# Optimization experiments

Measured on AMD Instinct MI355X. Metric: run time of the kernel, lower is better.

The kernel has to match this reference:

```python
import jax, jax.numpy as jnp
import numpy as np

N_NODES = 50000
N_EDGES = 1600000
DIM_IN = 64
DIM = 64
DIM_OUT = 32
N_GRAPHS = 64
DELTA = 2.5749
BN_EPS = 1e-5


def _lin(x, W, b):
    return x @ W.T + b


def _pna_conv(x, src, dst, mlp_W, mlp_b, W1, b1, W2, b2):
    # GINConv with overridden PNA aggregate: nn(x + aggr(x_j))
    msgs = x[src]                                               # [E, d]
    n = x.shape[0]
    sums = jax.ops.segment_sum(msgs, dst, num_segments=n)       # [N, d]
    maxs = jax.ops.segment_max(msgs, dst, num_segments=n)
    cnt = jax.ops.segment_sum(jnp.ones((msgs.shape[0], 1), msgs.dtype), dst,
                              num_segments=n)                   # [N, 1]
    means = sums / cnt
    var = jax.nn.relu(jax.ops.segment_sum(msgs * msgs, dst, num_segments=n) / cnt
                      - means * means)
    aggr = jnp.concatenate([sums, maxs, means, var], axis=1)    # [N, 4d]
    comb = jnp.concatenate([aggr, (cnt / DELTA) * aggr, (DELTA / cnt) * aggr],
                           axis=1)                              # [N, 12d]
    a = _lin(comb, mlp_W, mlp_b)                                # [N, d]
    h = x + a                                                   # (1+eps)*x + aggr, eps=0
    return _lin(jax.nn.relu(_lin(h, W1, b1)), W2, b2)


def _bn(x, g, b):
    # BatchNorm1d with batch statistics (training-mode stats, biased var)
    m = x.mean(axis=0)
    v = ((x - m) ** 2).mean(axis=0)
    return g * (x - m) / jnp.sqrt(v + BN_EPS) + b


def setup_inputs() -> dict:
    key = jax.random.key(0)
    ks = jax.random.split(key, 32)
    x = jax.random.normal(ks[0], (N_NODES, DIM_IN), dtype=jnp.float32)
    src = jax.random.randint(ks[1], (N_EDGES,), 0, N_NODES)
    dst = jax.random.randint(ks[2], (N_EDGES,), 0, N_NODES)
    # guarantee every node has >=1 incoming edge (original divides by bincount)
    dst = dst.at[:N_NODES].set(jnp.arange(N_NODES))
    edge_index = jnp.stack([src, dst]).astype(jnp.int32)
    batch = jnp.sort(jax.random.randint(ks[3], (N_NODES,), 0, N_GRAPHS)).astype(jnp.int32)

    def w(k, shape):
        return jax.random.normal(k, shape, dtype=jnp.float32) * 0.1

    d = {"x": x, "edge_index": edge_index, "batch": batch}
    i = 4
    for c in ("c1", "c2", "c3"):
        d[f"{c}_mlp_W"] = w(ks[i], (DIM, DIM * 12)); i += 1
        d[f"{c}_mlp_b"] = jnp.zeros((DIM,), jnp.float32)
        d[f"{c}_W1"] = w(ks[i], (DIM, DIM)); i += 1
        d[f"{c}_b1"] = jnp.zeros((DIM,), jnp.float32)
        d[f"{c}_W2"] = w(ks[i], (DIM, DIM)); i += 1
        d[f"{c}_b2"] = jnp.zeros((DIM,), jnp.float32)
    for b in ("bn1", "bn2", "bn3"):
        d[f"{b}_g"] = jnp.ones((DIM,), jnp.float32)
        d[f"{b}_b"] = jnp.zeros((DIM,), jnp.float32)
    d["fc1_W"] = w(ks[i], (DIM, DIM)); i += 1
    d["fc1_b"] = jnp.zeros((DIM,), jnp.float32)
    d["fc2_W"] = w(ks[i], (DIM_OUT, DIM)); i += 1
    d["fc2_b"] = jnp.zeros((DIM_OUT,), jnp.float32)
    return d


def reference(x, edge_index, batch,
              c1_mlp_W, c1_mlp_b, c1_W1, c1_b1, c1_W2, c1_b2, bn1_g, bn1_b,
              c2_mlp_W, c2_mlp_b, c2_W1, c2_b1, c2_W2, c2_b2, bn2_g, bn2_b,
              c3_mlp_W, c3_mlp_b, c3_W1, c3_b1, c3_W2, c3_b2, bn3_g, bn3_b,
              fc1_W, fc1_b, fc2_W, fc2_b):
    src, dst = edge_index[0], edge_index[1]
    h = jax.nn.relu(_pna_conv(x, src, dst, c1_mlp_W, c1_mlp_b, c1_W1, c1_b1, c1_W2, c1_b2))
    h = _bn(h, bn1_g, bn1_b)
    h = jax.nn.relu(_pna_conv(h, src, dst, c2_mlp_W, c2_mlp_b, c2_W1, c2_b1, c2_W2, c2_b2))
    h = _bn(h, bn2_g, bn2_b)
    h = jax.nn.relu(_pna_conv(h, src, dst, c3_mlp_W, c3_mlp_b, c3_W1, c3_b1, c3_W2, c3_b2))
    h = _bn(h, bn3_g, bn3_b)
    g = jax.ops.segment_sum(h, batch, num_segments=N_GRAPHS)   # global_add_pool
    g = jax.nn.relu(_lin(g, fc1_W, fc1_b))                     # dropout disabled (eval)
    g = _lin(g, fc2_W, fc2_b)
    return jax.nn.log_softmax(g, axis=-1)
```

## Files before the change

kernel.cpp:

```cpp
#include <hip/hip_runtime.h>

#define NN 50000
#define NE 1600000
#define DD 64
#define NGRAPH 64
#define DOUT 32
#define DELTA_F 2.5749f
#define BN_EPS_F 1e-5f

typedef unsigned short ushort;
typedef __attribute__((ext_vector_type(8))) short short8;
typedef __attribute__((ext_vector_type(4))) float floatx4;

static __device__ __forceinline__ float blo(unsigned u) {
    return __uint_as_float(u << 16);
}
static __device__ __forceinline__ float bhi(unsigned u) {
    return __uint_as_float(u & 0xFFFF0000u);
}
static __device__ __forceinline__ float bu2f(ushort u) {
    return __uint_as_float(((unsigned)u) << 16);
}
static __device__ __forceinline__ ushort f2bu(float f) {
    unsigned u = __float_as_uint(f);
    unsigned r = (u + 0x7FFF + ((u >> 16) & 1)) >> 16;
    return (ushort)r;
}
static __device__ __forceinline__ unsigned pk(float a, float b) {
    return ((unsigned)f2bu(b) << 16) | (unsigned)f2bu(a);
}

__global__ void k_prep(const float* __restrict__ x, ushort* __restrict__ XH,
                       const float* __restrict__ w0, const float* __restrict__ w1,
                       const float* __restrict__ w2,
                       const float* __restrict__ a0, const float* __restrict__ a1,
                       const float* __restrict__ a2, const float* __restrict__ a3,
                       const float* __restrict__ a4, const float* __restrict__ a5,
                       ushort* __restrict__ Wb, float* __restrict__ Wsm,
                       int* __restrict__ counts, float* __restrict__ bnstat,
                       float* __restrict__ gpool) {
    int i = blockIdx.x * 256 + threadIdx.x;
    if (i < NN) counts[i] = 0;
    if (i < 384) bnstat[i] = 0.f;
    if (i < NGRAPH * DD) gpool[i] = 0.f;
    if (i < NN * 16) {
        float4 v = *(const float4*)(x + (size_t)i * 4);
        ushort4 h;
        h.x = f2bu(v.x); h.y = f2bu(v.y); h.z = f2bu(v.z); h.w = f2bu(v.w);
        *(ushort4*)(XH + (size_t)i * 4) = h;
    }
    if (i < 3 * 65536) {
        int layer = i / 65536, r = i % 65536;
        const float* w = (layer == 0) ? w0 : ((layer == 1) ? w1 : w2);
        int c = r / 16384, r2 = r % 16384;
        int kb = r2 >> 11, r3 = r2 & 2047;
        int t = r3 >> 9, r4 = r3 & 511;
        int l = r4 >> 3, j = r4 & 7;
        int k = kb * 32 + (l >> 4) * 8 + j;
        int o = t * 16 + (l & 15);
        int g = (c == 0) ? 0 : ((c == 3) ? 2 : 1);
        float wv = w[o * 768 + g * 256 + k];
        ushort h = f2bu(wv);
        Wb[i] = (c == 2) ? f2bu(wv - bu2f(h)) : h;
    } else if (i < 3 * 65536 + 6 * 4096) {
        int r2 = i - 3 * 65536;
        int l = r2 >> 12, r = r2 & 4095;
        const float* w = (l == 0) ? a0 : (l == 1) ? a1 : (l == 2) ? a2
                       : (l == 3) ? a3 : (l == 4) ? a4 : a5;
        int o = r >> 6, j = r & 63;
        Wsm[l * 4096 + j * 64 + o] = w[r];
    }
}

__global__ void k_rank(const int* __restrict__ dst, int* __restrict__ counts,
                       int* __restrict__ rank) {
    int e = blockIdx.x * 256 + threadIdx.x;
    if (e < NE) rank[e] = atomicAdd(&counts[dst[e]], 1);
}

__global__ void k_scan_a(const int* __restrict__ counts, int* __restrict__ blockSums) {
    __shared__ int red[256];
    int tid = threadIdx.x;
    int gid = blockIdx.x * 256 + tid;
    int v = (gid < NN) ? counts[gid] : 0;
    red[tid] = v;
    __syncthreads();
    for (int s = 128; s > 0; s >>= 1) {
        if (tid < s) red[tid] += red[tid + s];
        __syncthreads();
    }
    if (tid == 0) blockSums[blockIdx.x] = red[0];
}

__global__ void k_scan_b(const int* __restrict__ blockSums, int* __restrict__ blockBase,
                         const int* __restrict__ batch, int* __restrict__ gcnt) {
    __shared__ int sh[256];
    int tid = threadIdx.x;
    int v = (tid < 196) ? blockSums[tid] : 0;
    sh[tid] = v;
    __syncthreads();
    for (int off = 1; off < 256; off <<= 1) {
        int t = (tid >= off) ? sh[tid - off] : 0;
        __syncthreads();
        sh[tid] += t;
        __syncthreads();
    }
    blockBase[tid] = sh[tid] - v;
    if (tid < NGRAPH) {
        auto lb = [&](int g) {
            int lo = 0, hi = NN;
            while (lo < hi) {
                int mid = (lo + hi) >> 1;
                if (batch[mid] < g) lo = mid + 1; else hi = mid;
            }
            return lo;
        };
        gcnt[tid] = lb(tid + 1) - lb(tid);
    }
}

__global__ void k_scan_c(const int* __restrict__ counts, const int* __restrict__ blockBase,
                         int* __restrict__ row_ptr) {
    __shared__ int sh[256];
    int tid = threadIdx.x;
    int gid = blockIdx.x * 256 + tid;
    int v = (gid < NN) ? counts[gid] : 0;
    sh[tid] = v;
    __syncthreads();
    for (int off = 1; off < 256; off <<= 1) {
        int t = (tid >= off) ? sh[tid - off] : 0;
        __syncthreads();
        sh[tid] += t;
        __syncthreads();
    }
    int excl = blockBase[blockIdx.x] + sh[tid] - v;
    if (gid <= NN) row_ptr[gid] = excl;
}

__global__ void k_place(const int* __restrict__ src, const int* __restrict__ dst,
                        const int* __restrict__ rank, const int* __restrict__ row_ptr,
                        int* __restrict__ csr_src) {
    int e = blockIdx.x * 256 + threadIdx.x;
    if (e < NE) csr_src[row_ptr[dst[e]] + rank[e]] = src[e];
}

#define MBIAS(i) aux[i]
#define B1V(i)   aux[64 + (i)]
#define B2V(i)   aux[128 + (i)]
#define DEGV(m)  aux[192 + (m)]
#define AFFS(i)  aux[224 + (i)]
#define AFFB(i)  aux[288 + (i)]

__global__ __launch_bounds__(256, 4) void k_fused(
    const ushort* __restrict__ XHin, ushort* __restrict__ XHout,
    const int* __restrict__ row_ptr, const int* __restrict__ csr_src,
    const ushort* __restrict__ Wbh,
    const float* __restrict__ mlp_b,
    const float* __restrict__ W1t, const float* __restrict__ b1,
    const float* __restrict__ W2t, const float* __restrict__ b2,
    const float* __restrict__ affstat, const float* __restrict__ affg,
    const float* __restrict__ affb,
    float* __restrict__ bnstat,
    const int* __restrict__ batch, float* __restrict__ gpool, int do_pool) {
    __shared__ __align__(16) char smem[27136];
    ushort* const Agh = (ushort*)smem;
    ushort* const Agl = (ushort*)(smem + 12800);
    float* const aux = (float*)(smem + 25600);
    int* const ibatch = (int*)(smem + 27008);
    float* const hsf = (float*)smem;

    const int tid = threadIdx.x;
    const int node0 = blockIdx.x * 32;

    if (tid < 64) {
        MBIAS(tid) = mlp_b[tid];
        B1V(tid) = b1[tid];
        B2V(tid) = b2[tid];
        float A = 1.f, Bv = 0.f;
        if (affstat) {
            float mean = affstat[tid] * (1.f / NN);
            float var = fmaxf(affstat[64 + tid] * (1.f / NN) - mean * mean, 0.f);
            float inv = rsqrtf(var + BN_EPS_F);
            A = affg[tid] * inv;
            Bv = affb[tid] - mean * A;
        }
        AFFS(tid) = A;
        AFFB(tid) = Bv;
    }
    if (tid < 32) {
        int node = node0 + tid;
        ibatch[tid] = (do_pool && node < NN) ? batch[node] : -1;
    }
    __syncthreads();

    {
        const int l8 = tid & 7;
        const int m = tid >> 3;
        const int node = node0 + m;
        const int f0 = l8 * 8;
        const ushort* Xp = XHin + f0;

        float s[8], q[8], mx[8];
#pragma unroll
        for (int i = 0; i < 8; ++i) { s[i] = 0.f; q[i] = 0.f; mx[i] = -3.402823466e38f; }

        auto acc8 = [&](const uint4& rr) {
            float v0 = blo(rr.x), v1 = bhi(rr.x);
            float v2 = blo(rr.y), v3 = bhi(rr.y);
            float v4 = blo(rr.z), v5 = bhi(rr.z);
            float v6 = blo(rr.w), v7 = bhi(rr.w);
            s[0] += v0; q[0] = fmaf(v0, v0, q[0]); mx[0] = fmaxf(mx[0], v0);
            s[1] += v1; q[1] = fmaf(v1, v1, q[1]); mx[1] = fmaxf(mx[1], v1);
            s[2] += v2; q[2] = fmaf(v2, v2, q[2]); mx[2] = fmaxf(mx[2], v2);
            s[3] += v3; q[3] = fmaf(v3, v3, q[3]); mx[3] = fmaxf(mx[3], v3);
            s[4] += v4; q[4] = fmaf(v4, v4, q[4]); mx[4] = fmaxf(mx[4], v4);
            s[5] += v5; q[5] = fmaf(v5, v5, q[5]); mx[5] = fmaxf(mx[5], v5);
            s[6] += v6; q[6] = fmaf(v6, v6, q[6]); mx[6] = fmaxf(mx[6], v6);
            s[7] += v7; q[7] = fmaf(v7, v7, q[7]); mx[7] = fmaxf(mx[7], v7);
        };

        int beg = 0, end = 0;
        if (node < NN) { beg = row_ptr[node]; end = row_ptr[node + 1]; }
        const int deg = end - beg;
        const int nb = (deg + 3) >> 2;

        uint4 ra[4], rb[4];
        int ia[4];
        if (nb > 0) {
#pragma unroll
            for (int j = 0; j < 4; ++j) {
                int e = beg + j;
                ia[j] = csr_src[(e < end) ? e : end - 1];
            }
#pragma unroll
            for (int j = 0; j < 4; ++j)
                ra[j] = *(const uint4*)(Xp + (size_t)ia[j] * 64);
            if (nb > 1) {
#pragma unroll
                for (int j = 0; j < 4; ++j) {
                    int e = beg + 4 + j;
                    ia[j] = csr_src[(e < end) ? e : end - 1];
                }
            }
        }
        for (int t = 0; t < nb; ++t) {
            if (t + 1 < nb) {
#pragma unroll
                for (int j = 0; j < 4; ++j)
                    rb[j] = *(const uint4*)(Xp + (size_t)ia[j] * 64);
            }
            if (t + 2 < nb) {
                int b2e = beg + (t + 2) * 4;
#pragma unroll
                for (int j = 0; j < 4; ++j) {
                    int e = b2e + j;
                    ia[j] = csr_src[(e < end) ? e : end - 1];
                }
            }
            int cnt = end - (beg + t * 4);
            if (cnt >= 4) {
#pragma unroll
                for (int j = 0; j < 4; ++j) acc8(ra[j]);
            } else {
#pragma unroll
                for (int j = 0; j < 4; ++j) if (j < cnt) acc8(ra[j]);
            }
            if (t + 1 < nb) {
#pragma unroll
                for (int j = 0; j < 4; ++j) ra[j] = rb[j];
            }
        }

        float cdeg = (node < NN) ? (float)deg : 1.f;
        float rc = 1.0f / cdeg;
        float var[8];
#pragma unroll
        for (int i = 0; i < 8; ++i) {
            float mean = s[i] * rc;
            var[i] = fmaxf(q[i] * rc - mean * mean, 0.f);
            if (node >= NN) { mx[i] = 0.f; var[i] = 0.f; }
        }
#pragma unroll
        for (int i = 0; i < 8; ++i) {
            float Af = AFFS(f0 + i), Bf = AFFB(f0 + i);
            s[i] = Af * s[i] + cdeg * Bf;
            mx[i] = Af * mx[i] + Bf;
            var[i] = Af * Af * var[i];
        }
        ushort* dh = Agh + m * 200 + f0;
        ushort* dl = Agl + m * 200 + f0;
        auto emit8 = [&](const float* v, int off) {
            ushort h0 = f2bu(v[0]), h1 = f2bu(v[1]), h2 = f2bu(v[2]), h3 = f2bu(v[3]);
            ushort h4 = f2bu(v[4]), h5 = f2bu(v[5]), h6 = f2bu(v[6]), h7 = f2bu(v[7]);
            uint4 hv;
            hv.x = (unsigned)h0 | ((unsigned)h1 << 16);
            hv.y = (unsigned)h2 | ((unsigned)h3 << 16);
            hv.z = (unsigned)h4 | ((unsigned)h5 << 16);
            hv.w = (unsigned)h6 | ((unsigned)h7 << 16);
            uint4 lv;
            lv.x = pk(v[0] - bu2f(h0), v[1] - bu2f(h1));
            lv.y = pk(v[2] - bu2f(h2), v[3] - bu2f(h3));
            lv.z = pk(v[4] - bu2f(h4), v[5] - bu2f(h5));
            lv.w = pk(v[6] - bu2f(h6), v[7] - bu2f(h7));
            *(uint4*)(dh + off) = hv;
            *(uint4*)(dl + off) = lv;
        };
        emit8(s, 0);
        emit8(mx, 64);
        emit8(var, 128);
        if (l8 == 0) DEGV(m) = cdeg;
    }
    __syncthreads();

    const int ln = tid & 63, wvi = tid >> 6;
    const int quad = ln >> 4, l16 = ln & 15;
    const int mtile = wvi >> 1;
    const int nt0 = (wvi & 1) * 2;

    const ushort* ArowH = Agh + (mtile * 16 + l16) * 200 + quad * 8;
    const ushort* ArowL = Agl + (mtile * 16 + l16) * 200 + quad * 8;
    short8 afh[6], afl[6];
#pragma unroll
    for (int i = 0; i < 6; ++i) {
        const int off = (i >> 1) * 64 + (i & 1) * 32;
        afh[i] = *(const short8*)(ArowH + off);
        afl[i] = *(const short8*)(ArowL + off);
    }
    __syncthreads();

#pragma unroll
    for (int nti = 0; nti < 2; ++nti) {
        const int nt = nt0 + nti;
        floatx4 aA0 = (floatx4){0.f, 0.f, 0.f, 0.f};
        floatx4 aB0 = (floatx4){0.f, 0.f, 0.f, 0.f};
        floatx4 aA1 = (floatx4){0.f, 0.f, 0.f, 0.f};
        floatx4 aB1 = (floatx4){0.f, 0.f, 0.f, 0.f};
        floatx4 aA2 = (floatx4){0.f, 0.f, 0.f, 0.f};
        floatx4 aB2 = (floatx4){0.f, 0.f, 0.f, 0.f};
#pragma unroll
        for (int kb = 0; kb < 8; ++kb) {
            const int am = (kb < 4) ? kb : ((kb < 6) ? (kb - 4) : (kb - 2));
            const int base = ((kb * 4 + nt) * 512) + ln * 8;
            short8 w0 = *(const short8*)(Wbh + base);
            short8 w1h = *(const short8*)(Wbh + 16384 + base);
            short8 w2 = *(const short8*)(Wbh + 3 * 16384 + base);
            if (kb == 4 || kb == 5) {
                aB0 = __builtin_amdgcn_mfma_f32_16x16x32_bf16(afh[am], w0, aB0, 0, 0, 0);
                aB1 = __builtin_amdgcn_mfma_f32_16x16x32_bf16(afh[am], w1h, aB1, 0, 0, 0);
                aB2 = __builtin_amdgcn_mfma_f32_16x16x32_bf16(afh[am], w2, aB2, 0, 0, 0);
            } else {
                short8 w1l = *(const short8*)(Wbh + 2 * 16384 + base);
                aA0 = __builtin_amdgcn_mfma_f32_16x16x32_bf16(afh[am], w0, aA0, 0, 0, 0);
                aA1 = __builtin_amdgcn_mfma_f32_16x16x32_bf16(afh[am], w1h, aA1, 0, 0, 0);
                aA1 = __builtin_amdgcn_mfma_f32_16x16x32_bf16(afl[am], w1h, aA1, 0, 0, 0);
                aA1 = __builtin_amdgcn_mfma_f32_16x16x32_bf16(afh[am], w1l, aA1, 0, 0, 0);
                aA2 = __builtin_amdgcn_mfma_f32_16x16x32_bf16(afh[am], w2, aA2, 0, 0, 0);
            }
        }
#pragma unroll
        for (int r = 0; r < 4; ++r) {
            int m = mtile * 16 + quad * 4 + r;
            float dg = DEGV(m), rcd = 1.f / dg;
            float cA2 = DELTA_F * rcd;
            float cB2 = DELTA_F * rcd * rcd;
            float cA1 = dg * (1.0f / DELTA_F);
            int n = nt * 16 + l16;
            hsf[n * 34 + m] = aA0[r] + rcd * aB0[r]
                            + cA2 * aA2[r] + cB2 * aB2[r]
                            + cA1 * aA1[r] + (1.0f / DELTA_F) * aB1[r];
        }
    }
    __syncthreads();

    const int tx = tid & 15, ty = tid >> 4;
    const int o0 = tx * 4, n0 = ty * 2;
#pragma unroll
    for (int ni = 0; ni < 2; ++ni) {
        int n = n0 + ni;
        int node = node0 + n;
        float xa4[4] = {0.f, 0.f, 0.f, 0.f};
        if (node < NN) {
            ushort4 hx = *(const ushort4*)(XHin + (size_t)node * DD + o0);
            xa4[0] = AFFS(o0 + 0) * bu2f(hx.x) + AFFB(o0 + 0);
            xa4[1] = AFFS(o0 + 1) * bu2f(hx.y) + AFFB(o0 + 1);
            xa4[2] = AFFS(o0 + 2) * bu2f(hx.z) + AFFB(o0 + 2);
            xa4[3] = AFFS(o0 + 3) * bu2f(hx.w) + AFFB(o0 + 3);
        }
#pragma unroll
        for (int oi = 0; oi < 4; ++oi) {
            int idx = (o0 + oi) * 34 + n;
            hsf[idx] = hsf[idx] + xa4[oi] + MBIAS(o0 + oi);
        }
    }
    __syncthreads();

    const float2* const hs2 = (const float2*)hsf;
    float l1[8];
#pragma unroll
    for (int i = 0; i < 8; ++i) l1[i] = 0.f;
#pragma unroll 4
    for (int j = 0; j < 64; ++j) {
        float2 a = hs2[j * 17 + ty];
        const float4 wv4 = *(const float4*)(W1t + j * 64 + o0);
        l1[0] += a.x * wv4.x; l1[1] += a.x * wv4.y; l1[2] += a.x * wv4.z; l1[3] += a.x * wv4.w;
        l1[4] += a.y * wv4.x; l1[5] += a.y * wv4.y; l1[6] += a.y * wv4.z; l1[7] += a.y * wv4.w;
    }
    __syncthreads();
#pragma unroll
    for (int ni = 0; ni < 2; ++ni)
#pragma unroll
        for (int oi = 0; oi < 4; ++oi)
            hsf[(o0 + oi) * 34 + n0 + ni] = fmaxf(l1[ni * 4 + oi] + B1V(o0 + oi), 0.f);
    __syncthreads();

    float l2[8];
#pragma unroll
    for (int i = 0; i < 8; ++i) l2[i] = 0.f;
#pragma unroll 4
    for (int j = 0; j < 64; ++j) {
        float2 a = hs2[j * 17 + ty];
        const float4 wv4 = *(const float4*)(W2t + j * 64 + o0);
        l2[0] += a.x * wv4.x; l2[1] += a.x * wv4.y; l2[2] += a.x * wv4.z; l2[3] += a.x * wv4.w;
        l2[4] += a.y * wv4.x; l2[5] += a.y * wv4.y; l2[6] += a.y * wv4.z; l2[7] += a.y * wv4.w;
    }
    __syncthreads();
#pragma unroll
    for (int ni = 0; ni < 2; ++ni) {
        int node = node0 + n0 + ni;
        float4 yv;
        yv.x = fmaxf(l2[ni * 4 + 0] + B2V(o0 + 0), 0.f);
        yv.y = fmaxf(l2[ni * 4 + 1] + B2V(o0 + 1), 0.f);
        yv.z = fmaxf(l2[ni * 4 + 2] + B2V(o0 + 2), 0.f);
        yv.w = fmaxf(l2[ni * 4 + 3] + B2V(o0 + 3), 0.f);
        if (node < NN && XHout) {
            ushort4 h;
            h.x = f2bu(yv.x); h.y = f2bu(yv.y);
            h.z = f2bu(yv.z); h.w = f2bu(yv.w);
            *(ushort4*)(XHout + (size_t)node * DD + o0) = h;
        }
        hsf[(o0 + 0) * 34 + n0 + ni] = yv.x;
        hsf[(o0 + 1) * 34 + n0 + ni] = yv.y;
        hsf[(o0 + 2) * 34 + n0 + ni] = yv.z;
        hsf[(o0 + 3) * 34 + n0 + ni] = yv.w;
    }
    __syncthreads();

    if (tid < 64) {
        float s = 0.f, sq = 0.f;
        float pacc = 0.f;
        int curg = ibatch[0];
        int lim = NN - node0;
        if (lim > 32) lim = 32;
        for (int n = 0; n < lim; ++n) {
            float v = hsf[tid * 34 + n];
            s += v;
            sq += v * v;
            if (do_pool) {
                int g = ibatch[n];
                if (g != curg) {
                    atomicAdd(&gpool[(size_t)curg * DD + tid], pacc);
                    pacc = 0.f;
                    curg = g;
                }
                pacc += v;
            }
        }
        if (do_pool && curg >= 0)
            atomicAdd(&gpool[(size_t)curg * DD + tid], pacc);
        atomicAdd(&bnstat[tid], s);
        atomicAdd(&bnstat[64 + tid], sq);
    }
}

__global__ __launch_bounds__(256) void k_head(const float* __restrict__ gpool,
                                              const float* __restrict__ bs3,
                                              const float* __restrict__ g3,
                                              const float* __restrict__ b3,
                                              const int* __restrict__ gcnt,
                                              const float* __restrict__ fc1W, const float* __restrict__ fc1b,
                                              const float* __restrict__ fc2W, const float* __restrict__ fc2b,
                                              float* __restrict__ out) {
    __shared__ float sh[12640];
    float* const gs = sh;
    float* const w1t = sh + 4096;
    float* const z1s = sh + 8256;
    float* const b1s = sh + 12416;
    float* const b2s = sh + 12480;
    float* const sc3 = sh + 12512;
    float* const shf3 = sh + 12576;
    float* const w2t = sh;
    float* const z2s = sh + 4096;

    int tid = threadIdx.x;
    if (tid < 64) {
        float mean = bs3[tid] * (1.f / NN);
        float var = fmaxf(bs3[64 + tid] * (1.f / NN) - mean * mean, 0.f);
        float inv = rsqrtf(var + BN_EPS_F);
        float A = g3[tid] * inv;
        sc3[tid] = A;
        shf3[tid] = b3[tid] - mean * A;
    }
    __syncthreads();
    for (int i = tid; i < 4096; i += 256) {
        int o = i >> 6, j = i & 63;
        gs[i] = sc3[j] * gpool[i] + shf3[j] * (float)gcnt[o];
        w1t[j * 65 + o] = fc1W[i];
    }
    if (tid < 64) b1s[tid] = fc1b[tid];
    if (tid < 32) b2s[tid] = fc2b[tid];
    __syncthreads();
    {
        int tx = tid & 15, ty = tid >> 4, o0 = tx * 4, g0 = ty * 4;
        float acc[16];
#pragma unroll
        for (int i = 0; i < 16; ++i) acc[i] = 0.f;
        for (int j = 0; j < 64; ++j) {
            float w0 = w1t[j * 65 + o0 + 0], w1 = w1t[j * 65 + o0 + 1];
            float w2 = w1t[j * 65 + o0 + 2], w3 = w1t[j * 65 + o0 + 3];
#pragma unroll
            for (int gi = 0; gi < 4; ++gi) {
                float a = gs[(g0 + gi) * 64 + j];
                acc[gi * 4 + 0] += a * w0; acc[gi * 4 + 1] += a * w1;
                acc[gi * 4 + 2] += a * w2; acc[gi * 4 + 3] += a * w3;
            }
        }
        __syncthreads();
#pragma unroll
        for (int gi = 0; gi < 4; ++gi)
#pragma unroll
            for (int oi = 0; oi < 4; ++oi)
                z1s[(g0 + gi) * 65 + o0 + oi] = fmaxf(acc[gi * 4 + oi] + b1s[o0 + oi], 0.f);
    }
    for (int i = tid; i < 2048; i += 256) {
        int o = i >> 6, j = i & 63;
        w2t[j * 33 + o] = fc2W[i];
    }
    __syncthreads();
    {
        int tx = tid & 7, ty = tid >> 3, o0 = tx * 4, g0 = ty * 2;
        float acc[8];
#pragma unroll
        for (int i = 0; i < 8; ++i) acc[i] = 0.f;
        for (int j = 0; j < 64; ++j) {
            float w0 = w2t[j * 33 + o0 + 0], w1 = w2t[j * 33 + o0 + 1];
            float w2 = w2t[j * 33 + o0 + 2], w3 = w2t[j * 33 + o0 + 3];
            float a0 = z1s[(g0 + 0) * 65 + j];
            float a1 = z1s[(g0 + 1) * 65 + j];
            acc[0] += a0 * w0; acc[1] += a0 * w1; acc[2] += a0 * w2; acc[3] += a0 * w3;
            acc[4] += a1 * w0; acc[5] += a1 * w1; acc[6] += a1 * w2; acc[7] += a1 * w3;
        }
#pragma unroll
        for (int gi = 0; gi < 2; ++gi)
#pragma unroll
            for (int oi = 0; oi < 4; ++oi)
                z2s[(g0 + gi) * 33 + o0 + oi] = acc[gi * 4 + oi] + b2s[o0 + oi];
    }
    __syncthreads();
    if (tid < 64) {
        float m = -3.402823466e38f;
        for (int c = 0; c < DOUT; ++c) m = fmaxf(m, z2s[tid * 33 + c]);
        float s = 0.f;
        for (int c = 0; c < DOUT; ++c) s += expf(z2s[tid * 33 + c] - m);
        float lse = m + logf(s);
        for (int c = 0; c < DOUT; ++c)
            out[tid * DOUT + c] = z2s[tid * 33 + c] - lse;
    }
}

extern "C" void kernel_launch(void* const* d_in, const int* in_sizes, int n_in,
                              void* d_out, int out_size, void* d_ws, size_t ws_size,
                              hipStream_t stream) {
    const float* x = (const float*)d_in[0];
    const int* ei = (const int*)d_in[1];
    const int* src = ei;
    const int* dst = ei + NE;
    const int* batch = (const int*)d_in[2];
    const float *mlpW[3], *mlpB[3], *w1[3], *bb1[3], *w2[3], *bb2[3], *bng[3], *bnb[3];
    for (int l = 0; l < 3; ++l) {
        mlpW[l] = (const float*)d_in[3 + 6 * l];
        mlpB[l] = (const float*)d_in[4 + 6 * l];
        w1[l]   = (const float*)d_in[5 + 6 * l];
        bb1[l]  = (const float*)d_in[6 + 6 * l];
        w2[l]   = (const float*)d_in[7 + 6 * l];
        bb2[l]  = (const float*)d_in[8 + 6 * l];
        bng[l]  = (const float*)d_in[21 + 2 * l];
        bnb[l]  = (const float*)d_in[22 + 2 * l];
    }
    const float* fc1W = (const float*)d_in[27];
    const float* fc1b = (const float*)d_in[28];
    const float* fc2W = (const float*)d_in[29];
    const float* fc2b = (const float*)d_in[30];
    float* out = (float*)d_out;

    char* ws = (char*)d_ws;
    size_t off = 0;
    auto alloc = [&](size_t bytes) -> void* {
        void* p = ws + off;
        off = (off + bytes + 511) & ~(size_t)511;
        return p;
    };
    int* counts    = (int*)alloc((size_t)NN * 4);
    int* row_ptr   = (int*)alloc((size_t)(NN + 1) * 4);
    int* rank      = (int*)alloc((size_t)NE * 4);
    int* blockSums = (int*)alloc(256 * 4);
    int* blockBase = (int*)alloc(256 * 4);
    int* csr_src   = (int*)alloc((size_t)NE * 4);
    ushort* XHA    = (ushort*)alloc((size_t)NN * DD * 2);
    ushort* XHB    = (ushort*)alloc((size_t)NN * DD * 2);
    ushort* Wb     = (ushort*)alloc((size_t)3 * 65536 * 2);
    float* Wsm     = (float*)alloc((size_t)6 * 4096 * 4);
    float* bnstat  = (float*)alloc(384 * 4);
    float* gpool   = (float*)alloc((size_t)NGRAPH * DD * 4);
    int* gcnt      = (int*)alloc(NGRAPH * 4);
    (void)ws_size; (void)in_sizes; (void)n_in; (void)out_size;

    k_prep<<<3125, 256, 0, stream>>>(x, XHA,
                                     mlpW[0], mlpW[1], mlpW[2],
                                     w1[0], w2[0], w1[1], w2[1], w1[2], w2[2],
                                     Wb, Wsm, counts, bnstat, gpool);
    k_rank<<<6250, 256, 0, stream>>>(dst, counts, rank);
    k_scan_a<<<196, 256, 0, stream>>>(counts, blockSums);
    k_scan_b<<<1, 256, 0, stream>>>(blockSums, blockBase, batch, gcnt);
    k_scan_c<<<196, 256, 0, stream>>>(counts, blockBase, row_ptr);
    k_place<<<6250, 256, 0, stream>>>(src, dst, rank, row_ptr, csr_src);

    k_fused<<<1563, 256, 0, stream>>>(XHA, XHB, row_ptr, csr_src,
                                      Wb, mlpB[0],
                                      Wsm, bb1[0], Wsm + 4096, bb2[0],
                                      nullptr, nullptr, nullptr,
                                      bnstat, batch, gpool, 0);
    k_fused<<<1563, 256, 0, stream>>>(XHB, XHA, row_ptr, csr_src,
                                      Wb + 65536, mlpB[1],
                                      Wsm + 2 * 4096, bb1[1], Wsm + 3 * 4096, bb2[1],
                                      bnstat, bng[0], bnb[0],
                                      bnstat + 128, batch, gpool, 0);
    k_fused<<<1563, 256, 0, stream>>>(XHA, nullptr, row_ptr, csr_src,
                                      Wb + 2 * 65536, mlpB[2],
                                      Wsm + 4 * 4096, bb1[2], Wsm + 5 * 4096, bb2[2],
                                      bnstat + 128, bng[1], bnb[1],
                                      bnstat + 256, batch, gpool, 1);
    k_head<<<1, 256, 0, stream>>>(gpool, bnstat + 256, bng[2], bnb[2], gcnt,
                                  fc1W, fc1b, fc2W, fc2b, out);
}
```

Baseline: 493.4 us.

## Double threads per fused block and vectorize edge rank/place kernels

```diff
diff --git a/kernel.cpp b/kernel.cpp
--- a/kernel.cpp
+++ b/kernel.cpp
@@ -74,8 +74,16 @@
 
 __global__ void k_rank(const int* __restrict__ dst, int* __restrict__ counts,
                        int* __restrict__ rank) {
-    int e = blockIdx.x * 256 + threadIdx.x;
-    if (e < NE) rank[e] = atomicAdd(&counts[dst[e]], 1);
+    int i = blockIdx.x * 256 + threadIdx.x;
+    if (i < NE / 4) {
+        int4 d = ((const int4*)dst)[i];
+        int4 r;
+        r.x = atomicAdd(&counts[d.x], 1);
+        r.y = atomicAdd(&counts[d.y], 1);
+        r.z = atomicAdd(&counts[d.z], 1);
+        r.w = atomicAdd(&counts[d.w], 1);
+        ((int4*)rank)[i] = r;
+    }
 }
 
 __global__ void k_scan_a(const int* __restrict__ counts, int* __restrict__ blockSums) {
@@ -140,8 +148,16 @@
 __global__ void k_place(const int* __restrict__ src, const int* __restrict__ dst,
                         const int* __restrict__ rank, const int* __restrict__ row_ptr,
                         int* __restrict__ csr_src) {
-    int e = blockIdx.x * 256 + threadIdx.x;
-    if (e < NE) csr_src[row_ptr[dst[e]] + rank[e]] = src[e];
+    int i = blockIdx.x * 256 + threadIdx.x;
+    if (i < NE / 4) {
+        int4 s4 = ((const int4*)src)[i];
+        int4 d4 = ((const int4*)dst)[i];
+        int4 r4 = ((const int4*)rank)[i];
+        csr_src[row_ptr[d4.x] + r4.x] = s4.x;
+        csr_src[row_ptr[d4.y] + r4.y] = s4.y;
+        csr_src[row_ptr[d4.z] + r4.z] = s4.z;
+        csr_src[row_ptr[d4.w] + r4.w] = s4.w;
+    }
 }
 
 #define MBIAS(i) aux[i]
@@ -151,7 +167,7 @@
 #define AFFS(i)  aux[224 + (i)]
 #define AFFB(i)  aux[288 + (i)]
 
-__global__ __launch_bounds__(256, 4) void k_fused(
+__global__ __launch_bounds__(512, 6) void k_fused(
     const ushort* __restrict__ XHin, ushort* __restrict__ XHout,
     const int* __restrict__ row_ptr, const int* __restrict__ csr_src,
     const ushort* __restrict__ Wbh,
@@ -194,29 +210,23 @@
     __syncthreads();
 
     {
-        const int l8 = tid & 7;
-        const int m = tid >> 3;
+        const int l16g = tid & 15;
+        const int m = tid >> 4;
         const int node = node0 + m;
-        const int f0 = l8 * 8;
+        const int f0 = l16g * 4;
         const ushort* Xp = XHin + f0;
 
-        float s[8], q[8], mx[8];
-#pragma unroll
-        for (int i = 0; i < 8; ++i) { s[i] = 0.f; q[i] = 0.f; mx[i] = -3.402823466e38f; }
-
-        auto acc8 = [&](const uint4& rr) {
+        float s[4], q[4], mx[4];
+#pragma unroll
+        for (int i = 0; i < 4; ++i) { s[i] = 0.f; q[i] = 0.f; mx[i] = -3.402823466e38f; }
+
+        auto acc4 = [&](const uint2& rr) {
             float v0 = blo(rr.x), v1 = bhi(rr.x);
             float v2 = blo(rr.y), v3 = bhi(rr.y);
-            float v4 = blo(rr.z), v5 = bhi(rr.z);
-            float v6 = blo(rr.w), v7 = bhi(rr.w);
             s[0] += v0; q[0] = fmaf(v0, v0, q[0]); mx[0] = fmaxf(mx[0], v0);
             s[1] += v1; q[1] = fmaf(v1, v1, q[1]); mx[1] = fmaxf(mx[1], v1);
             s[2] += v2; q[2] = fmaf(v2, v2, q[2]); mx[2] = fmaxf(mx[2], v2);
             s[3] += v3; q[3] = fmaf(v3, v3, q[3]); mx[3] = fmaxf(mx[3], v3);
-            s[4] += v4; q[4] = fmaf(v4, v4, q[4]); mx[4] = fmaxf(mx[4], v4);
-            s[5] += v5; q[5] = fmaf(v5, v5, q[5]); mx[5] = fmaxf(mx[5], v5);
-            s[6] += v6; q[6] = fmaf(v6, v6, q[6]); mx[6] = fmaxf(mx[6], v6);
-            s[7] += v7; q[7] = fmaf(v7, v7, q[7]); mx[7] = fmaxf(mx[7], v7);
         };
 
         int beg = 0, end = 0;
@@ -224,7 +234,7 @@
         const int deg = end - beg;
         const int nb = (deg + 3) >> 2;
 
-        uint4 ra[4], rb[4];
+        uint2 ra[4], rb[4];
         int ia[4];
         if (nb > 0) {
 #pragma unroll
@@ -234,7 +244,7 @@
             }
 #pragma unroll
             for (int j = 0; j < 4; ++j)
-                ra[j] = *(const uint4*)(Xp + (size_t)ia[j] * 64);
+                ra[j] = *(const uint2*)(Xp + (size_t)ia[j] * 64);
             if (nb > 1) {
 #pragma unroll
                 for (int j = 0; j < 4; ++j) {
@@ -247,7 +257,7 @@
             if (t + 1 < nb) {
 #pragma unroll
                 for (int j = 0; j < 4; ++j)
-                    rb[j] = *(const uint4*)(Xp + (size_t)ia[j] * 64);
+                    rb[j] = *(const uint2*)(Xp + (size_t)ia[j] * 64);
             }
             if (t + 2 < nb) {
                 int b2e = beg + (t + 2) * 4;
@@ -260,10 +270,10 @@
             int cnt = end - (beg + t * 4);
             if (cnt >= 4) {
 #pragma unroll
-                for (int j = 0; j < 4; ++j) acc8(ra[j]);
+                for (int j = 0; j < 4; ++j) acc4(ra[j]);
             } else {
 #pragma unroll
-                for (int j = 0; j < 4; ++j) if (j < cnt) acc8(ra[j]);
+                for (int j = 0; j < 4; ++j) if (j < cnt) acc4(ra[j]);
             }
             if (t + 1 < nb) {
 #pragma unroll
@@ -273,15 +283,15 @@
 
         float cdeg = (node < NN) ? (float)deg : 1.f;
         float rc = 1.0f / cdeg;
-        float var[8];
-#pragma unroll
-        for (int i = 0; i < 8; ++i) {
+        float var[4];
+#pragma unroll
+        for (int i = 0; i < 4; ++i) {
             float mean = s[i] * rc;
             var[i] = fmaxf(q[i] * rc - mean * mean, 0.f);
             if (node >= NN) { mx[i] = 0.f; var[i] = 0.f; }
         }
 #pragma unroll
-        for (int i = 0; i < 8; ++i) {
+        for (int i = 0; i < 4; ++i) {
             float Af = AFFS(f0 + i), Bf = AFFB(f0 + i);
             s[i] = Af * s[i] + cdeg * Bf;
             mx[i] = Af * mx[i] + Bf;
@@ -289,48 +299,40 @@
         }
         ushort* dh = Agh + m * 200 + f0;
         ushort* dl = Agl + m * 200 + f0;
-        auto emit8 = [&](const float* v, int off) {
+        auto emit4 = [&](const float* v, int off) {
             ushort h0 = f2bu(v[0]), h1 = f2bu(v[1]), h2 = f2bu(v[2]), h3 = f2bu(v[3]);
-            ushort h4 = f2bu(v[4]), h5 = f2bu(v[5]), h6 = f2bu(v[6]), h7 = f2bu(v[7]);
-            uint4 hv;
+            uint2 hv;
             hv.x = (unsigned)h0 | ((unsigned)h1 << 16);
             hv.y = (unsigned)h2 | ((unsigned)h3 << 16);
-            hv.z = (unsigned)h4 | ((unsigned)h5 << 16);
-            hv.w = (unsigned)h6 | ((unsigned)h7 << 16);
-            uint4 lv;
+            uint2 lv;
             lv.x = pk(v[0] - bu2f(h0), v[1] - bu2f(h1));
             lv.y = pk(v[2] - bu2f(h2), v[3] - bu2f(h3));
-            lv.z = pk(v[4] - bu2f(h4), v[5] - bu2f(h5));
-            lv.w = pk(v[6] - bu2f(h6), v[7] - bu2f(h7));
-            *(uint4*)(dh + off) = hv;
-            *(uint4*)(dl + off) = lv;
+            *(uint2*)(dh + off) = hv;
+            *(uint2*)(dl + off) = lv;
         };
-        emit8(s, 0);
-        emit8(mx, 64);
-        emit8(var, 128);
-        if (l8 == 0) DEGV(m) = cdeg;
+        emit4(s, 0);
+        emit4(mx, 64);
+        emit4(var, 128);
+        if (l16g == 0) DEGV(m) = cdeg;
     }
     __syncthreads();
 
     const int ln = tid & 63, wvi = tid >> 6;
     const int quad = ln >> 4, l16 = ln & 15;
-    const int mtile = wvi >> 1;
-    const int nt0 = (wvi & 1) * 2;
+    const int mtile = wvi >> 2;
+    const int nt = wvi & 3;
 
     const ushort* ArowH = Agh + (mtile * 16 + l16) * 200 + quad * 8;
     const ushort* ArowL = Agl + (mtile * 16 + l16) * 200 + quad * 8;
-    short8 afh[6], afl[6];
+    short8 afh[6];
 #pragma unroll
     for (int i = 0; i < 6; ++i) {
         const int off = (i >> 1) * 64 + (i & 1) * 32;
         afh[i] = *(const short8*)(ArowH + off);
-        afl[i] = *(const short8*)(ArowL + off);
-    }
-    __syncthreads();
-
-#pragma unroll
-    for (int nti = 0; nti < 2; ++nti) {
-        const int nt = nt0 + nti;
+    }
+    __syncthreads();
+
+    {
         floatx4 aA0 = (floatx4){0.f, 0.f, 0.f, 0.f};
         floatx4 aB0 = (floatx4){0.f, 0.f, 0.f, 0.f};
         floatx4 aA1 = (floatx4){0.f, 0.f, 0.f, 0.f};
@@ -350,9 +352,10 @@
                 aB2 = __builtin_amdgcn_mfma_f32_16x16x32_bf16(afh[am], w2, aB2, 0, 0, 0);
             } else {
                 short8 w1l = *(const short8*)(Wbh + 2 * 16384 + base);
+                short8 al = *(const short8*)(ArowL + ((am >> 1) * 64 + (am & 1) * 32));
                 aA0 = __builtin_amdgcn_mfma_f32_16x16x32_bf16(afh[am], w0, aA0, 0, 0, 0);
                 aA1 = __builtin_amdgcn_mfma_f32_16x16x32_bf16(afh[am], w1h, aA1, 0, 0, 0);
-                aA1 = __builtin_amdgcn_mfma_f32_16x16x32_bf16(afl[am], w1h, aA1, 0, 0, 0);
+                aA1 = __builtin_amdgcn_mfma_f32_16x16x32_bf16(al, w1h, aA1, 0, 0, 0);
                 aA1 = __builtin_amdgcn_mfma_f32_16x16x32_bf16(afh[am], w1l, aA1, 0, 0, 0);
                 aA2 = __builtin_amdgcn_mfma_f32_16x16x32_bf16(afh[am], w2, aA2, 0, 0, 0);
             }
@@ -373,11 +376,9 @@
     __syncthreads();
 
     const int tx = tid & 15, ty = tid >> 4;
-    const int o0 = tx * 4, n0 = ty * 2;
-#pragma unroll
-    for (int ni = 0; ni < 2; ++ni) {
-        int n = n0 + ni;
-        int node = node0 + n;
+    const int o0 = tx * 4;
+    {
+        int node = node0 + ty;
         float xa4[4] = {0.f, 0.f, 0.f, 0.f};
         if (node < NN) {
             ushort4 hx = *(const ushort4*)(XHin + (size_t)node * DD + o0);
@@ -388,60 +389,54 @@
         }
 #pragma unroll
         for (int oi = 0; oi < 4; ++oi) {
-            int idx = (o0 + oi) * 34 + n;
+            int idx = (o0 + oi) * 34 + ty;
             hsf[idx] = hsf[idx] + xa4[oi] + MBIAS(o0 + oi);
         }
     }
     __syncthreads();
 
-    const float2* const hs2 = (const float2*)hsf;
-    float l1[8];
-#pragma unroll
-    for (int i = 0; i < 8; ++i) l1[i] = 0.f;
+    float l1[4];
+#pragma unroll
+    for (int i = 0; i < 4; ++i) l1[i] = 0.f;
 #pragma unroll 4
     for (int j = 0; j < 64; ++j) {
-        float2 a = hs2[j * 17 + ty];
+        float a = hsf[j * 34 + ty];
         const float4 wv4 = *(const float4*)(W1t + j * 64 + o0);
-        l1[0] += a.x * wv4.x; l1[1] += a.x * wv4.y; l1[2] += a.x * wv4.z; l1[3] += a.x * wv4.w;
-        l1[4] += a.y * wv4.x; l1[5] += a.y * wv4.y; l1[6] += a.y * wv4.z; l1[7] += a.y * wv4.w;
-    }
-    __syncthreads();
-#pragma unroll
-    for (int ni = 0; ni < 2; ++ni)
-#pragma unroll
-        for (int oi = 0; oi < 4; ++oi)
-            hsf[(o0 + oi) * 34 + n0 + ni] = fmaxf(l1[ni * 4 + oi] + B1V(o0 + oi), 0.f);
-    __syncthreads();
-
-    float l2[8];
-#pragma unroll
-    for (int i = 0; i < 8; ++i) l2[i] = 0.f;
+        l1[0] += a * wv4.x; l1[1] += a * wv4.y; l1[2] += a * wv4.z; l1[3] += a * wv4.w;
+    }
+    __syncthreads();
+#pragma unroll
+    for (int oi = 0; oi < 4; ++oi)
+        hsf[(o0 + oi) * 34 + ty] = fmaxf(l1[oi] + B1V(o0 + oi), 0.f);
+    __syncthreads();
+
+    float l2[4];
+#pragma unroll
+    for (int i = 0; i < 4; ++i) l2[i] = 0.f;
 #pragma unroll 4
     for (int j = 0; j < 64; ++j) {
-        float2 a = hs2[j * 17 + ty];
+        float a = hsf[j * 34 + ty];
         const float4 wv4 = *(const float4*)(W2t + j * 64 + o0);
-        l2[0] += a.x * wv4.x; l2[1] += a.x * wv4.y; l2[2] += a.x * wv4.z; l2[3] += a.x * wv4.w;
-        l2[4] += a.y * wv4.x; l2[5] += a.y * wv4.y; l2[6] += a.y * wv4.z; l2[7] += a.y * wv4.w;
-    }
-    __syncthreads();
-#pragma unroll
-    for (int ni = 0; ni < 2; ++ni) {
-        int node = node0 + n0 + ni;
+        l2[0] += a * wv4.x; l2[1] += a * wv4.y; l2[2] += a * wv4.z; l2[3] += a * wv4.w;
+    }
+    __syncthreads();
+    {
+        int node = node0 + ty;
         float4 yv;
-        yv.x = fmaxf(l2[ni * 4 + 0] + B2V(o0 + 0), 0.f);
-        yv.y = fmaxf(l2[ni * 4 + 1] + B2V(o0 + 1), 0.f);
-        yv.z = fmaxf(l2[ni * 4 + 2] + B2V(o0 + 2), 0.f);
-        yv.w = fmaxf(l2[ni * 4 + 3] + B2V(o0 + 3), 0.f);
+        yv.x = fmaxf(l2[0] + B2V(o0 + 0), 0.f);
+        yv.y = fmaxf(l2[1] + B2V(o0 + 1), 0.f);
+        yv.z = fmaxf(l2[2] + B2V(o0 + 2), 0.f);
+        yv.w = fmaxf(l2[3] + B2V(o0 + 3), 0.f);
         if (node < NN && XHout) {
             ushort4 h;
             h.x = f2bu(yv.x); h.y = f2bu(yv.y);
             h.z = f2bu(yv.z); h.w = f2bu(yv.w);
             *(ushort4*)(XHout + (size_t)node * DD + o0) = h;
         }
-        hsf[(o0 + 0) * 34 + n0 + ni] = yv.x;
-        hsf[(o0 + 1) * 34 + n0 + ni] = yv.y;
-        hsf[(o0 + 2) * 34 + n0 + ni] = yv.z;
-        hsf[(o0 + 3) * 34 + n0 + ni] = yv.w;
+        hsf[(o0 + 0) * 34 + ty] = yv.x;
+        hsf[(o0 + 1) * 34 + ty] = yv.y;
+        hsf[(o0 + 2) * 34 + ty] = yv.z;
+        hsf[(o0 + 3) * 34 + ty] = yv.w;
     }
     __syncthreads();
 
@@ -618,23 +613,23 @@
                                      mlpW[0], mlpW[1], mlpW[2],
                                      w1[0], w2[0], w1[1], w2[1], w1[2], w2[2],
                                      Wb, Wsm, counts, bnstat, gpool);
-    k_rank<<<6250, 256, 0, stream>>>(dst, counts, rank);
+    k_rank<<<1563, 256, 0, stream>>>(dst, counts, rank);
     k_scan_a<<<196, 256, 0, stream>>>(counts, blockSums);
     k_scan_b<<<1, 256, 0, stream>>>(blockSums, blockBase, batch, gcnt);
     k_scan_c<<<196, 256, 0, stream>>>(counts, blockBase, row_ptr);
-    k_place<<<6250, 256, 0, stream>>>(src, dst, rank, row_ptr, csr_src);
-
-    k_fused<<<1563, 256, 0, stream>>>(XHA, XHB, row_ptr, csr_src,
+    k_place<<<1563, 256, 0, stream>>>(src, dst, rank, row_ptr, csr_src);
+
+    k_fused<<<1563, 512, 0, stream>>>(XHA, XHB, row_ptr, csr_src,
                                       Wb, mlpB[0],
                                       Wsm, bb1[0], Wsm + 4096, bb2[0],
                                       nullptr, nullptr, nullptr,
                                       bnstat, batch, gpool, 0);
-    k_fused<<<1563, 256, 0, stream>>>(XHB, XHA, row_ptr, csr_src,
+    k_fused<<<1563, 512, 0, stream>>>(XHB, XHA, row_ptr, csr_src,
                                       Wb + 65536, mlpB[1],
                                       Wsm + 2 * 4096, bb1[1], Wsm + 3 * 4096, bb2[1],
                                       bnstat, bng[0], bnb[0],
                                       bnstat + 128, batch, gpool, 0);
-    k_fused<<<1563, 256, 0, stream>>>(XHA, nullptr, row_ptr, csr_src,
+    k_fused<<<1563, 512, 0, stream>>>(XHA, nullptr, row_ptr, csr_src,
                                       Wb + 2 * 65536, mlpB[2],
                                       Wsm + 4 * 4096, bb1[2], Wsm + 5 * 4096, bb2[2],
                                       bnstat + 128, bng[1], bnb[1],
```

Measured after the change: 555.4 us. 1.13x slower.

## Move node MLP linears to split-bf16 MFMA and vectorize edge CSR build

Applied to the files above, without the earlier changes.

```diff
diff --git a/kernel.cpp b/kernel.cpp
--- a/kernel.cpp
+++ b/kernel.cpp
@@ -36,7 +36,7 @@
                        const float* __restrict__ a0, const float* __restrict__ a1,
                        const float* __restrict__ a2, const float* __restrict__ a3,
                        const float* __restrict__ a4, const float* __restrict__ a5,
-                       ushort* __restrict__ Wb, float* __restrict__ Wsm,
+                       ushort* __restrict__ Wb, ushort* __restrict__ Wsb,
                        int* __restrict__ counts, float* __restrict__ bnstat,
                        float* __restrict__ gpool) {
     int i = blockIdx.x * 256 + threadIdx.x;
@@ -62,20 +62,37 @@
         float wv = w[o * 768 + g * 256 + k];
         ushort h = f2bu(wv);
         Wb[i] = (c == 2) ? f2bu(wv - bu2f(h)) : h;
-    } else if (i < 3 * 65536 + 6 * 4096) {
-        int r2 = i - 3 * 65536;
-        int l = r2 >> 12, r = r2 & 4095;
-        const float* w = (l == 0) ? a0 : (l == 1) ? a1 : (l == 2) ? a2
-                       : (l == 3) ? a3 : (l == 4) ? a4 : a5;
-        int o = r >> 6, j = r & 63;
-        Wsm[l * 4096 + j * 64 + o] = w[r];
+    } else if (i < 3 * 65536 + 3 * 16384) {
+        int i2 = i - 3 * 65536;
+        int layer = i2 / 16384, r = i2 % 16384;
+        int lin = r >> 13, r2 = r & 8191;
+        int hl = r2 >> 12, r3 = r2 & 4095;
+        int kb = r3 >> 11, r4 = r3 & 2047;
+        int t = r4 >> 9, r5 = r4 & 511;
+        int l = r5 >> 3, j = r5 & 7;
+        int k = kb * 32 + (l >> 4) * 8 + j;
+        int o = t * 16 + (l & 15);
+        const float* w = (lin == 0)
+            ? ((layer == 0) ? a0 : (layer == 1) ? a2 : a4)
+            : ((layer == 0) ? a1 : (layer == 1) ? a3 : a5);
+        float wv = w[o * 64 + k];
+        ushort h = f2bu(wv);
+        Wsb[i2] = hl ? f2bu(wv - bu2f(h)) : h;
     }
 }
 
 __global__ void k_rank(const int* __restrict__ dst, int* __restrict__ counts,
                        int* __restrict__ rank) {
-    int e = blockIdx.x * 256 + threadIdx.x;
-    if (e < NE) rank[e] = atomicAdd(&counts[dst[e]], 1);
+    int i = blockIdx.x * 256 + threadIdx.x;
+    if (i < NE / 4) {
+        int4 d = ((const int4*)dst)[i];
+        int4 r;
+        r.x = atomicAdd(&counts[d.x], 1);
+        r.y = atomicAdd(&counts[d.y], 1);
+        r.z = atomicAdd(&counts[d.z], 1);
+        r.w = atomicAdd(&counts[d.w], 1);
+        ((int4*)rank)[i] = r;
+    }
 }
 
 __global__ void k_scan_a(const int* __restrict__ counts, int* __restrict__ blockSums) {
@@ -140,8 +157,16 @@
 __global__ void k_place(const int* __restrict__ src, const int* __restrict__ dst,
                         const int* __restrict__ rank, const int* __restrict__ row_ptr,
                         int* __restrict__ csr_src) {
-    int e = blockIdx.x * 256 + threadIdx.x;
-    if (e < NE) csr_src[row_ptr[dst[e]] + rank[e]] = src[e];
+    int i = blockIdx.x * 256 + threadIdx.x;
+    if (i < NE / 4) {
+        int4 s4 = ((const int4*)src)[i];
+        int4 d4 = ((const int4*)dst)[i];
+        int4 r4 = ((const int4*)rank)[i];
+        csr_src[row_ptr[d4.x] + r4.x] = s4.x;
+        csr_src[row_ptr[d4.y] + r4.y] = s4.y;
+        csr_src[row_ptr[d4.z] + r4.z] = s4.z;
+        csr_src[row_ptr[d4.w] + r4.w] = s4.w;
+    }
 }
 
 #define MBIAS(i) aux[i]
@@ -154,10 +179,9 @@
 __global__ __launch_bounds__(256, 4) void k_fused(
     const ushort* __restrict__ XHin, ushort* __restrict__ XHout,
     const int* __restrict__ row_ptr, const int* __restrict__ csr_src,
-    const ushort* __restrict__ Wbh,
+    const ushort* __restrict__ Wbh, const ushort* __restrict__ Wlin,
     const float* __restrict__ mlp_b,
-    const float* __restrict__ W1t, const float* __restrict__ b1,
-    const float* __restrict__ W2t, const float* __restrict__ b2,
+    const float* __restrict__ b1, const float* __restrict__ b2,
     const float* __restrict__ affstat, const float* __restrict__ affg,
     const float* __restrict__ affb,
     float* __restrict__ bnstat,
@@ -394,56 +418,91 @@
     }
     __syncthreads();
 
-    const float2* const hs2 = (const float2*)hsf;
-    float l1[8];
-#pragma unroll
-    for (int i = 0; i < 8; ++i) l1[i] = 0.f;
-#pragma unroll 4
-    for (int j = 0; j < 64; ++j) {
-        float2 a = hs2[j * 17 + ty];
-        const float4 wv4 = *(const float4*)(W1t + j * 64 + o0);
-        l1[0] += a.x * wv4.x; l1[1] += a.x * wv4.y; l1[2] += a.x * wv4.z; l1[3] += a.x * wv4.w;
-        l1[4] += a.y * wv4.x; l1[5] += a.y * wv4.y; l1[6] += a.y * wv4.z; l1[7] += a.y * wv4.w;
-    }
-    __syncthreads();
-#pragma unroll
-    for (int ni = 0; ni < 2; ++ni)
-#pragma unroll
-        for (int oi = 0; oi < 4; ++oi)
-            hsf[(o0 + oi) * 34 + n0 + ni] = fmaxf(l1[ni * 4 + oi] + B1V(o0 + oi), 0.f);
-    __syncthreads();
-
-    float l2[8];
-#pragma unroll
-    for (int i = 0; i < 8; ++i) l2[i] = 0.f;
-#pragma unroll 4
-    for (int j = 0; j < 64; ++j) {
-        float2 a = hs2[j * 17 + ty];
-        const float4 wv4 = *(const float4*)(W2t + j * 64 + o0);
-        l2[0] += a.x * wv4.x; l2[1] += a.x * wv4.y; l2[2] += a.x * wv4.z; l2[3] += a.x * wv4.w;
-        l2[4] += a.y * wv4.x; l2[5] += a.y * wv4.y; l2[6] += a.y * wv4.z; l2[7] += a.y * wv4.w;
-    }
-    __syncthreads();
-#pragma unroll
-    for (int ni = 0; ni < 2; ++ni) {
-        int node = node0 + n0 + ni;
-        float4 yv;
-        yv.x = fmaxf(l2[ni * 4 + 0] + B2V(o0 + 0), 0.f);
-        yv.y = fmaxf(l2[ni * 4 + 1] + B2V(o0 + 1), 0.f);
-        yv.z = fmaxf(l2[ni * 4 + 2] + B2V(o0 + 2), 0.f);
-        yv.w = fmaxf(l2[ni * 4 + 3] + B2V(o0 + 3), 0.f);
-        if (node < NN && XHout) {
-            ushort4 h;
-            h.x = f2bu(yv.x); h.y = f2bu(yv.y);
-            h.z = f2bu(yv.z); h.w = f2bu(yv.w);
-            *(ushort4*)(XHout + (size_t)node * DD + o0) = h;
-        }
-        hsf[(o0 + 0) * 34 + n0 + ni] = yv.x;
-        hsf[(o0 + 1) * 34 + n0 + ni] = yv.y;
-        hsf[(o0 + 2) * 34 + n0 + ni] = yv.z;
-        hsf[(o0 + 3) * 34 + n0 + ni] = yv.w;
-    }
-    __syncthreads();
+    {
+        floatx4 lacc[2];
+        lacc[0] = (floatx4){0.f, 0.f, 0.f, 0.f};
+        lacc[1] = (floatx4){0.f, 0.f, 0.f, 0.f};
+#pragma unroll
+        for (int kb = 0; kb < 2; ++kb) {
+            short8 ah, al;
+#pragma unroll
+            for (int j = 0; j < 8; ++j) {
+                float v = hsf[(kb * 32 + quad * 8 + j) * 34 + mtile * 16 + l16];
+                ushort h = f2bu(v);
+                ah[j] = (short)h;
+                al[j] = (short)f2bu(v - bu2f(h));
+            }
+#pragma unroll
+            for (int nti = 0; nti < 2; ++nti) {
+                const int boff = ((kb * 4 + nt0 + nti) * 512) + ln * 8;
+                short8 wh = *(const short8*)(Wlin + boff);
+                short8 wl = *(const short8*)(Wlin + 4096 + boff);
+                lacc[nti] = __builtin_amdgcn_mfma_f32_16x16x32_bf16(ah, wh, lacc[nti], 0, 0, 0);
+                lacc[nti] = __builtin_amdgcn_mfma_f32_16x16x32_bf16(al, wh, lacc[nti], 0, 0, 0);
+                lacc[nti] = __builtin_amdgcn_mfma_f32_16x16x32_bf16(ah, wl, lacc[nti], 0, 0, 0);
+            }
+        }
+        __syncthreads();
+#pragma unroll
+        for (int nti = 0; nti < 2; ++nti) {
+            int o = (nt0 + nti) * 16 + l16;
+#pragma unroll
+            for (int r = 0; r < 4; ++r)
+                hsf[o * 34 + mtile * 16 + quad * 4 + r] = fmaxf(lacc[nti][r] + B1V(o), 0.f);
+        }
+    }
+    __syncthreads();
+
+    {
+        floatx4 lacc[2];
+        lacc[0] = (floatx4){0.f, 0.f, 0.f, 0.f};
+        lacc[1] = (floatx4){0.f, 0.f, 0.f, 0.f};
+#pragma unroll
+        for (int kb = 0; kb < 2; ++kb) {
+            short8 ah, al;
+#pragma unroll
+            for (int j = 0; j < 8; ++j) {
+                float v = hsf[(kb * 32 + quad * 8 + j) * 34 + mtile * 16 + l16];
+                ushort h = f2bu(v);
+                ah[j] = (short)h;
+                al[j] = (short)f2bu(v - bu2f(h));
+            }
+#pragma unroll
+            for (int nti = 0; nti < 2; ++nti) {
+                const int boff = ((kb * 4 + nt0 + nti) * 512) + ln * 8;
+                short8 wh = *(const short8*)(Wlin + 8192 + boff);
+                short8 wl = *(const short8*)(Wlin + 12288 + boff);
+                lacc[nti] = __builtin_amdgcn_mfma_f32_16x16x32_bf16(ah, wh, lacc[nti], 0, 0, 0);
+                lacc[nti] = __builtin_amdgcn_mfma_f32_16x16x32_bf16(al, wh, lacc[nti], 0, 0, 0);
+                lacc[nti] = __builtin_amdgcn_mfma_f32_16x16x32_bf16(ah, wl, lacc[nti], 0, 0, 0);
+            }
+        }
+        __syncthreads();
+#pragma unroll
+        for (int nti = 0; nti < 2; ++nti) {
+            int o = (nt0 + nti) * 16 + l16;
+#pragma unroll
+            for (int r = 0; r < 4; ++r)
+                hsf[o * 34 + mtile * 16 + quad * 4 + r] = fmaxf(lacc[nti][r] + B2V(o), 0.f);
+        }
+    }
+    __syncthreads();
+
+    if (XHout) {
+#pragma unroll
+        for (int ni = 0; ni < 2; ++ni) {
+            int n = n0 + ni;
+            int node = node0 + n;
+            if (node < NN) {
+                ushort4 h;
+                h.x = f2bu(hsf[(o0 + 0) * 34 + n]);
+                h.y = f2bu(hsf[(o0 + 1) * 34 + n]);
+                h.z = f2bu(hsf[(o0 + 2) * 34 + n]);
+                h.w = f2bu(hsf[(o0 + 3) * 34 + n]);
+                *(ushort4*)(XHout + (size_t)node * DD + o0) = h;
+            }
+        }
+    }
 
     if (tid < 64) {
         float s = 0.f, sq = 0.f;
@@ -608,7 +667,7 @@
     ushort* XHA    = (ushort*)alloc((size_t)NN * DD * 2);
     ushort* XHB    = (ushort*)alloc((size_t)NN * DD * 2);
     ushort* Wb     = (ushort*)alloc((size_t)3 * 65536 * 2);
-    float* Wsm     = (float*)alloc((size_t)6 * 4096 * 4);
+    ushort* Wsb    = (ushort*)alloc((size_t)3 * 16384 * 2);
     float* bnstat  = (float*)alloc(384 * 4);
     float* gpool   = (float*)alloc((size_t)NGRAPH * DD * 4);
     int* gcnt      = (int*)alloc(NGRAPH * 4);
@@ -617,26 +676,23 @@
     k_prep<<<3125, 256, 0, stream>>>(x, XHA,
                                      mlpW[0], mlpW[1], mlpW[2],
                                      w1[0], w2[0], w1[1], w2[1], w1[2], w2[2],
-                                     Wb, Wsm, counts, bnstat, gpool);
-    k_rank<<<6250, 256, 0, stream>>>(dst, counts, rank);
+                                     Wb, Wsb, counts, bnstat, gpool);
+    k_rank<<<1563, 256, 0, stream>>>(dst, counts, rank);
     k_scan_a<<<196, 256, 0, stream>>>(counts, blockSums);
     k_scan_b<<<1, 256, 0, stream>>>(blockSums, blockBase, batch, gcnt);
     k_scan_c<<<196, 256, 0, stream>>>(counts, blockBase, row_ptr);
-    k_place<<<6250, 256, 0, stream>>>(src, dst, rank, row_ptr, csr_src);
+    k_place<<<1563, 256, 0, stream>>>(src, dst, rank, row_ptr, csr_src);
 
     k_fused<<<1563, 256, 0, stream>>>(XHA, XHB, row_ptr, csr_src,
-                                      Wb, mlpB[0],
-                                      Wsm, bb1[0], Wsm + 4096, bb2[0],
+                                      Wb, Wsb, mlpB[0], bb1[0], bb2[0],
                                       nullptr, nullptr, nullptr,
                                       bnstat, batch, gpool, 0);
     k_fused<<<1563, 256, 0, stream>>>(XHB, XHA, row_ptr, csr_src,
-                                      Wb + 65536, mlpB[1],
-                                      Wsm + 2 * 4096, bb1[1], Wsm + 3 * 4096, bb2[1],
+                                      Wb + 65536, Wsb + 16384, mlpB[1], bb1[1], bb2[1],
                                       bnstat, bng[0], bnb[0],
                                       bnstat + 128, batch, gpool, 0);
     k_fused<<<1563, 256, 0, stream>>>(XHA, nullptr, row_ptr, csr_src,
-                                      Wb + 2 * 65536, mlpB[2],
-                                      Wsm + 4 * 4096, bb1[2], Wsm + 5 * 4096, bb2[2],
+                                      Wb + 2 * 65536, Wsb + 2 * 16384, mlpB[2], bb1[2], bb2[2],
                                       bnstat + 128, bng[1], bnb[1],
                                       bnstat + 256, batch, gpool, 1);
     k_head<<<1, 256, 0, stream>>>(gpool, bnstat + 256, bng[2], bnb[2], gcnt,
```

Measured after the change: 467.2 us. 5.3% less time.
